# Kernel tuning notes

Hardware: AMD Instinct MI355X
Metric: run time of the kernel (lower is better)

## Reference

```python
import jax, jax.numpy as jnp
import numpy as np

H = 8       # num_heads
K = 16      # neighbours
LN_EPS = 1e-6

def _knn_indices(coords, k):
    # coords: (B,N,3) float32. Squared-euclidean distances preserve kNN ordering of cdist.
    d2 = jnp.sum(coords * coords, axis=-1)                      # (B,N)
    dist2 = d2[:, :, None] + d2[:, None, :] - 2.0 * jnp.einsum('bnd,bmd->bnm', coords, coords)
    _, idx = jax.lax.top_k(-dist2, k)                           # (B,N,k) smallest distances
    return idx

def _gather(x, idx):
    # x: (B,N,D), idx: (B,N,K) -> (B,N,K,D)
    return jax.vmap(lambda a, i: a[i])(x, idx)

def setup_inputs() -> dict:
    key = jax.random.key(0)
    ks = jax.random.split(key, 16)
    B, N, D = 2, 8192, 256
    P = 6
    std = 0.02
    inp = {
        'features': jax.random.normal(ks[0], (B, N, D), jnp.float32),
        'coords': jax.random.uniform(ks[1], (B, N, 3), jnp.float32),
        'normals': jax.random.normal(ks[2], (B, N, 3), jnp.float32),
        'mask': jnp.ones((B, N), jnp.float32),
        # linear weights stored (in, out): y = x @ W + b
        'Wq': jax.random.normal(ks[3], (D, D), jnp.float32) * std,
        'bq': jnp.zeros((D,), jnp.float32),
        'Wk': jax.random.normal(ks[4], (D, D), jnp.float32) * std,
        'bk': jnp.zeros((D,), jnp.float32),
        'Wv': jax.random.normal(ks[5], (D, D), jnp.float32) * std,
        'bv': jnp.zeros((D,), jnp.float32),
        'Wo': jax.random.normal(ks[6], (D, D), jnp.float32) * std,  # torch inits this to zero; random here for nontrivial test
        'bo': jnp.zeros((D,), jnp.float32),
        'Wp1': jax.random.normal(ks[7], (P, D), jnp.float32) * std,
        'bp1': jnp.zeros((D,), jnp.float32),
        'Wp2': jax.random.normal(ks[8], (D, D), jnp.float32) * std,
        'bp2': jnp.zeros((D,), jnp.float32),
        'gamma': jnp.ones((D,), jnp.float32),
        'beta': jnp.zeros((D,), jnp.float32),
    }
    return inp

def reference(features, coords, normals, mask, Wq, bq, Wk, bk, Wv, bv, Wo, bo,
              Wp1, bp1, Wp2, bp2, gamma, beta):
    B, N, D = features.shape
    dh = D // H
    scale = 1.0 / np.sqrt(dh).astype(np.float32)
    residual = features

    idx = _knn_indices(jax.lax.stop_gradient(coords), K)        # (B,N,K), no-grad as in torch

    nb_coords = _gather(coords, idx)                            # (B,N,K,3)
    rel_pos = coords[:, :, None, :] - nb_coords                 # (B,N,K,3)
    pos_input = jnp.concatenate(
        [rel_pos, jnp.broadcast_to(normals[:, :, None, :], rel_pos.shape)], axis=-1)  # (B,N,K,6)
    # pos MLP: Linear -> GELU(exact, torch default) -> Linear
    pos_emb = jax.nn.gelu(pos_input @ Wp1 + bp1, approximate=False) @ Wp2 + bp2       # (B,N,K,D)

    q = features @ Wq + bq                                      # (B,N,D)
    kp = features @ Wk + bk
    vp = features @ Wv + bv
    kg = _gather(kp, idx)                                       # (B,N,K,D)
    vg = _gather(vp, idx)

    k_comb = (kg + pos_emb).reshape(B, N, K, H, dh)
    v_comb = (vg + pos_emb).reshape(B, N, K, H, dh)
    qh = q.reshape(B, N, H, dh)

    logits = jnp.einsum('bnhd,bnkhd->bnkh', qh, k_comb) * scale  # (B,N,K,H)
    nb_valid = _gather(mask[..., None], idx)[..., 0]             # (B,N,K)
    logits = jnp.where(nb_valid[..., None] > 0, logits, -jnp.inf)
    attn = jax.nn.softmax(logits, axis=2)
    attn = jnp.nan_to_num(attn, nan=0.0)

    out = jnp.einsum('bnkh,bnkhd->bnhd', attn, v_comb).reshape(B, N, D)
    out = (out @ Wo + bo) * mask[..., None]

    h = residual + out
    mu = jnp.mean(h, axis=-1, keepdims=True)
    var = jnp.mean((h - mu) ** 2, axis=-1, keepdims=True)
    h = (h - mu) / jnp.sqrt(var + LN_EPS) * gamma + beta
    return h * mask[..., None]
```

## Files before the change

### kernel.cpp

```cpp
#include <hip/hip_runtime.h>
#include <hip/hip_bf16.h>
#include <math.h>

typedef unsigned short u16t;
typedef unsigned int   u32t;
typedef unsigned long long u64t;
typedef __attribute__((ext_vector_type(8))) short  short8;
typedef __attribute__((ext_vector_type(4))) float  floatx4;

#define NPTS   8192
#define DMODEL 256
#define BNTOT  16384
#define HSTR   264

__device__ __forceinline__ float bitsf(u32t u){ union { u32t i; float f; } v; v.i = u; return v.f; }
__device__ __forceinline__ float b2f(u16t s){ return bitsf(((u32t)s) << 16); }
__device__ __forceinline__ u16t f2b(float f){
  __hip_bfloat16 h = __float2bfloat16(f);
  return *reinterpret_cast<u16t*>(&h);
}
__device__ __forceinline__ uint4 pack8(const float* o){
  uint4 st;
  st.x = (u32t)f2b(o[0]) | ((u32t)f2b(o[1]) << 16);
  st.y = (u32t)f2b(o[2]) | ((u32t)f2b(o[3]) << 16);
  st.z = (u32t)f2b(o[4]) | ((u32t)f2b(o[5]) << 16);
  st.w = (u32t)f2b(o[6]) | ((u32t)f2b(o[7]) << 16);
  return st;
}

__device__ __forceinline__ float gelu_fast(float x){
  float ax = fabsf(x) * 0.70710678118654752f;
  float t  = __builtin_amdgcn_rcpf(__builtin_fmaf(0.3275911f, ax, 1.0f));
  float p  = t*(0.254829592f + t*(-0.284496736f + t*(1.421413741f +
             t*(-1.453152027f + t*1.061405429f))));
  float er = __builtin_fmaf(-p, __expf(-ax*ax), 1.0f);
  return 0.5f * x * (1.0f + copysignf(er, x));
}

__global__ __launch_bounds__(256) void fill_valf(float* p, int n, float v){
  int i = blockIdx.x * 256 + threadIdx.x;
  if (i < n) p[i] = v;
}

__global__ __launch_bounds__(256) void wprep4(const float* __restrict__ Wk,
                                              const float* __restrict__ Wv,
                                              const float* __restrict__ Wp2,
                                              const float* __restrict__ Wq,
                                              u16t* __restrict__ out) {
  int e = blockIdx.x * 256 + threadIdx.x;
  int m = e >> 16, r = e & 65535;
  const float* W = (m == 0) ? Wk : (m == 1 ? Wv : (m == 2 ? Wp2 : Wq));
  int v = r & 7, l = (r >> 3) & 63, cca = (r >> 9) & 15, ic = r >> 13;
  int i = ic * 32 + (l >> 4) * 8 + v;
  int c = cca * 16 + (l & 15);
  out[e] = f2b(W[(size_t)i * DMODEL + c]);
}
__global__ __launch_bounds__(256) void wprep1(const float* __restrict__ W,
                                              u16t* __restrict__ out) {
  int r = blockIdx.x * 256 + threadIdx.x;
  int v = r & 7, l = (r >> 3) & 63, cca = (r >> 9) & 15, ic = r >> 13;
  int i = ic * 32 + (l >> 4) * 8 + v;
  int c = cca * 16 + (l & 15);
  out[r] = f2b(W[(size_t)i * DMODEL + c]);
}

__device__ __forceinline__ void cswap_asc(u64t& a, u64t& b){
  u64t mn = (a < b) ? a : b;
  u64t mx = (a < b) ? b : a;
  a = mn; b = mx;
}
__device__ __forceinline__ void bitonic16(u64t v[16]){
  #pragma unroll
  for (int k = 2; k <= 16; k <<= 1) {
    #pragma unroll
    for (int j = k >> 1; j > 0; j >>= 1) {
      #pragma unroll
      for (int i = 0; i < 16; ++i) {
        int l = i ^ j;
        if (l > i) {
          if ((i & k) == 0) cswap_asc(v[i], v[l]);
          else              cswap_asc(v[l], v[i]);
        }
      }
    }
  }
}
__device__ __forceinline__ void merge16(u64t best[16], u64t v[16]){
  #pragma unroll
  for (int i = 0; i < 16; ++i) {
    u64t o = v[15 - i];
    best[i] = (best[i] < o) ? best[i] : o;
  }
  #pragma unroll
  for (int j = 8; j > 0; j >>= 1) {
    #pragma unroll
    for (int i = 0; i < 16; ++i) {
      int l = i ^ j;
      if (l > i) cswap_asc(best[i], best[l]);
    }
  }
}
__device__ __forceinline__ void knn_flush(u64t best[16], float& thrf, int& cnt,
                                          const u64t* bufw, int lane){
  u64t v[16];
  #pragma unroll
  for (int s = 0; s < 16; ++s) {
    u64t x = bufw[s * 64 + lane];
    v[s] = (s < cnt) ? x : 0xFFFFFFFFFFFFFFFFULL;
  }
  bitonic16(v);
  merge16(best, v);
  u32t k15 = (u32t)(best[15] >> 32);
  thrf = (k15 == 0xFFFFFFFFu) ? 3.3e38f
       : bitsf((k15 & 0x80000000u) ? (k15 ^ 0x80000000u) : ~k15);
  cnt = 0;
}

__global__ __launch_bounds__(256) void knn_partial(const float* __restrict__ coords,
                                                   u64t* __restrict__ pk) {
  int qb = blockIdx.x >> 3, ch = blockIdx.x & 7;
  int tid = threadIdx.x;
  int lane = tid & 63, wv = tid >> 6;
  int g = qb * 256 + tid;
  int b = g >> 13;
  alignas(16) __shared__ float4 tile[256];
  __shared__ u64t buf[4][16][64];

  float qx = coords[(size_t)g * 3 + 0];
  float qy = coords[(size_t)g * 3 + 1];
  float qz = coords[(size_t)g * 3 + 2];
  float qd2 = __fadd_rn(__fadd_rn(__fmul_rn(qx,qx), __fmul_rn(qy,qy)), __fmul_rn(qz,qz));

  u64t best[16];
  #pragma unroll
  for (int s = 0; s < 16; ++s) best[s] = 0xFFFFFFFFFFFFFFFFULL;
  float thrf = 3.3e38f;
  int  cnt = 0;
  u64t* bufw = &buf[wv][0][0];

  int cs = ch * 1024;
  for (int t = 0; t < 4; ++t) {
    int ci = cs + t * 256 + tid;
    size_t cb = (size_t)(b * NPTS + ci) * 3;
    float x = coords[cb + 0];
    float y = coords[cb + 1];
    float z = coords[cb + 2];
    float d2 = __fadd_rn(__fadd_rn(__fmul_rn(x,x), __fmul_rn(y,y)), __fmul_rn(z,z));
    __syncthreads();
    tile[tid] = make_float4(x, y, z, d2);
    __syncthreads();
    int cbase = cs + t * 256;
    for (int u = 0; u < 256; ++u) {
      float4 cd = tile[u];
      float dot = __fadd_rn(__fadd_rn(__fmul_rn(qx,cd.x), __fmul_rn(qy,cd.y)), __fmul_rn(qz,cd.z));
      float dist = __fsub_rn(__fadd_rn(qd2, cd.w), __fmul_rn(2.0f, dot));
      if (dist <= thrf) {
        u32t db  = __float_as_uint(dist);
        u32t key = db ^ ((u32t)(((int)db) >> 31) | 0x80000000u);
        bufw[cnt * 64 + lane] = ((u64t)key << 32) | (u32t)(cbase + u);
        ++cnt;
      }
      if (__any(cnt == 16)) knn_flush(best, thrf, cnt, bufw, lane);
    }
  }
  if (__any(cnt > 0)) knn_flush(best, thrf, cnt, bufw, lane);

  size_t base = (size_t)g * 128 + ch * 16;
  #pragma unroll
  for (int s = 0; s < 16; ++s) pk[base + s] = best[s];
}

__global__ __launch_bounds__(256) void knn_merge(const u64t* __restrict__ pk,
                                                 u16t* __restrict__ idxb) {
  int g = blockIdx.x * 256 + threadIdx.x;
  size_t base = (size_t)g * 128;
  int h[8];
  #pragma unroll
  for (int c = 0; c < 8; ++c) h[c] = 0;
  for (int s = 0; s < 16; ++s) {
    u64t bk = 0xFFFFFFFFFFFFFFFFULL; int bc = 0;
    #pragma unroll
    for (int c = 0; c < 8; ++c) {
      if (h[c] < 16) {
        u64t kk = pk[base + c * 16 + h[c]];
        if (kk < bk) { bk = kk; bc = c; }
      }
    }
    idxb[(size_t)g * 16 + s] = (u16t)(bk & 0xFFFFu);
    h[bc]++;
  }
}

__global__ __launch_bounds__(256) void gemm_kv_mfma(const float* __restrict__ feat,
    const u16t* __restrict__ frags,
    const float* __restrict__ bk, const float* __restrict__ bv,
    u16t* __restrict__ kb, u16t* __restrict__ vb) {
  int rbase = blockIdx.x * 32;
  int tid = threadIdx.x, lane = tid & 63, wvi = tid >> 6;
  int quad = lane >> 4, l15 = lane & 15;
  int mat = wvi >> 1, rg = wvi & 1;

  alignas(16) __shared__ u16t featS[32 * HSTR];

  {
    int r = tid >> 3, c0 = (tid & 7) * 32;
    const float* src = feat + (size_t)(rbase + r) * DMODEL + c0;
    u16t* dst = featS + r * HSTR + c0;
    #pragma unroll
    for (int t = 0; t < 4; ++t) {
      float4 a = *(const float4*)(src + t * 8);
      float4 b = *(const float4*)(src + t * 8 + 4);
      float o[8] = {a.x, a.y, a.z, a.w, b.x, b.y, b.z, b.w};
      *(uint4*)(dst + t * 8) = pack8(o);
    }
  }
  __syncthreads();

  short8 af[8];
  #pragma unroll
  for (int ic = 0; ic < 8; ++ic)
    af[ic] = *(const short8*)(featS + (rg * 16 + l15) * HSTR + ic * 32 + quad * 8);

  const u16t* wf    = frags + (size_t)mat * 65536;
  const float* bias = mat ? bv : bk;
  u16t* out         = mat ? vb : kb;

  floatx4 acc[16];
  #pragma unroll
  for (int ct = 0; ct < 16; ++ct) acc[ct] = (floatx4){0.f, 0.f, 0.f, 0.f};

  #pragma unroll
  for (int ic = 0; ic < 8; ++ic) {
    #pragma unroll
    for (int ct = 0; ct < 16; ++ct) {
      short8 bf = *(const short8*)(wf + (((size_t)(ic * 16 + ct) * 64 + lane) << 3));
      acc[ct] = __builtin_amdgcn_mfma_f32_16x16x32_bf16(af[ic], bf, acc[ct], 0, 0, 0);
    }
  }

  #pragma unroll
  for (int ct = 0; ct < 16; ++ct) {
    int col = ct * 16 + l15;
    float bvv = bias[col];
    #pragma unroll
    for (int r = 0; r < 4; ++r) {
      int row = rbase + rg * 16 + quad * 4 + r;
      out[(size_t)row * DMODEL + col] = f2b(acc[ct][r] + bvv);
    }
  }
}

__global__ __launch_bounds__(256, 4) void attn_mega(
    const float* __restrict__ coords, const float* __restrict__ normals,
    const float* __restrict__ maskp, const float* __restrict__ feat,
    const float* __restrict__ bq,
    const float* __restrict__ Wp1, const float* __restrict__ bp1,
    const float* __restrict__ bp2,
    const u16t* __restrict__ idxp,
    const u16t* __restrict__ wqfrag, const u16t* __restrict__ wp2frag,
    const u16t* __restrict__ kbuf, const u16t* __restrict__ vbuf,
    float* __restrict__ outp) {
  alignas(16) __shared__ u16t hemb[64 * HSTR];
  alignas(16) __shared__ u16t qB[8 * HSTR];
  __shared__ float wS[64];
  __shared__ int   idS[64];

  int c    = threadIdx.x;
  int lane = c & 63;
  int wv   = c >> 6;
  int quad = lane >> 4;
  int l15  = lane & 15;
  int wv4  = wv * 4;
  int qbase = blockIdx.x * 8;

  {
    int r = c >> 5, c0 = (c & 31) * 8;
    const float* src = feat + (size_t)(qbase + r) * DMODEL + c0;
    float4 a = *(const float4*)(src);
    float4 b = *(const float4*)(src + 4);
    float o[8] = {a.x, a.y, a.z, a.w, b.x, b.y, b.z, b.w};
    *(uint4*)(hemb + r * HSTR + c0) = pack8(o);
    uint4 z; z.x = 0u; z.y = 0u; z.z = 0u; z.w = 0u;
    *(uint4*)(hemb + (8 + r) * HSTR + c0) = z;
  }
  __syncthreads();

  {
    floatx4 qa[4];
    #pragma unroll
    for (int cc = 0; cc < 4; ++cc) qa[cc] = (floatx4){0.f, 0.f, 0.f, 0.f};
    #pragma unroll
    for (int ic = 0; ic < 8; ++ic) {
      short8 af = *(const short8*)(hemb + l15 * HSTR + ic * 32 + quad * 8);
      #pragma unroll
      for (int cc = 0; cc < 4; ++cc) {
        short8 bf = *(const short8*)(wqfrag + (((size_t)(ic * 16 + wv4 + cc) * 64 + lane) << 3));
        qa[cc] = __builtin_amdgcn_mfma_f32_16x16x32_bf16(af, bf, qa[cc], 0, 0, 0);
      }
    }
    if (quad < 2) {
      #pragma unroll
      for (int cc = 0; cc < 4; ++cc) {
        int col = (wv4 + cc) * 16 + l15;
        float bqv = bq[col];
        #pragma unroll
        for (int r = 0; r < 4; ++r)
          qB[(quad * 4 + r) * HSTR + col] = f2b(qa[cc][r] + bqv);
      }
    }
  }

  float w1[6];
  #pragma unroll
  for (int p = 0; p < 6; ++p) w1[p] = Wp1[p * DMODEL + c];
  float b1v = bp1[c];
  float b2c[4];
  #pragma unroll
  for (int cc = 0; cc < 4; ++cc) b2c[cc] = bp2[(wv4 + cc) * 16 + l15];
  const float lsc = 0.17677669529663687f;
  __syncthreads();

  #pragma unroll
  for (int G = 0; G < 2; ++G) {
    for (int ql = 0; ql < 4; ++ql) {
      int g = qbase + G * 4 + ql;
      int bb0 = (g >> 13) * NPTS;
      float qx = coords[(size_t)g * 3 + 0];
      float qy = coords[(size_t)g * 3 + 1];
      float qz = coords[(size_t)g * 3 + 2];
      float n0 = normals[(size_t)g * 3 + 0];
      float n1 = normals[(size_t)g * 3 + 1];
      float n2 = normals[(size_t)g * 3 + 2];
      #pragma unroll
      for (int j = 0; j < 16; ++j) {
        int id = (int)idxp[(size_t)g * 16 + j];
        size_t cb = (size_t)(bb0 + id) * 3;
        float rx = qx - coords[cb + 0];
        float ry = qy - coords[cb + 1];
        float rz = qz - coords[cb + 2];
        float pre = b1v + rx * w1[0] + ry * w1[1] + rz * w1[2]
                        + n0 * w1[3] + n1 * w1[4] + n2 * w1[5];
        hemb[(ql * 16 + j) * HSTR + c] = f2b(gelu_fast(pre));
      }
    }
    __syncthreads();

    floatx4 acc[4][4];
    #pragma unroll
    for (int rt = 0; rt < 4; ++rt)
      #pragma unroll
      for (int cc = 0; cc < 4; ++cc) acc[rt][cc] = (floatx4){0.f, 0.f, 0.f, 0.f};

    #pragma unroll
    for (int ic = 0; ic < 8; ++ic) {
      short8 af0 = *(const short8*)(hemb + ( 0 + l15) * HSTR + ic * 32 + quad * 8);
      short8 af1 = *(const short8*)(hemb + (16 + l15) * HSTR + ic * 32 + quad * 8);
      short8 af2 = *(const short8*)(hemb + (32 + l15) * HSTR + ic * 32 + quad * 8);
      short8 af3 = *(const short8*)(hemb + (48 + l15) * HSTR + ic * 32 + quad * 8);
      #pragma unroll
      for (int cc = 0; cc < 4; ++cc) {
        short8 bf = *(const short8*)(wp2frag + (((size_t)(ic * 16 + wv4 + cc) * 64 + lane) << 3));
        acc[0][cc] = __builtin_amdgcn_mfma_f32_16x16x32_bf16(af0, bf, acc[0][cc], 0, 0, 0);
        acc[1][cc] = __builtin_amdgcn_mfma_f32_16x16x32_bf16(af1, bf, acc[1][cc], 0, 0, 0);
        acc[2][cc] = __builtin_amdgcn_mfma_f32_16x16x32_bf16(af2, bf, acc[2][cc], 0, 0, 0);
        acc[3][cc] = __builtin_amdgcn_mfma_f32_16x16x32_bf16(af3, bf, acc[3][cc], 0, 0, 0);
      }
    }
    __syncthreads();
    #pragma unroll
    for (int rt = 0; rt < 4; ++rt)
      #pragma unroll
      for (int cc = 0; cc < 4; ++cc) {
        int cg = (wv4 + cc) * 16 + l15;
        #pragma unroll
        for (int r = 0; r < 4; ++r)
          hemb[(rt * 16 + quad * 4 + r) * HSTR + cg] = f2b(acc[rt][cc][r] + b2c[cc]);
      }
    __syncthreads();

    {
      int g = qbase + G * 4 + wv;
      int bb0 = (g >> 13) * NPTS;
      int idl = (int)idxp[(size_t)g * 16 + l15];
      float mvl = maskp[bb0 + idl];
      unsigned long long bm = __ballot(mvl > 0.0f);
      if (quad == 0) idS[wv * 16 + l15] = idl;
      const u16t* krow = kbuf + (size_t)(bb0 + idl) * DMODEL;
      const u16t* erow = hemb + (wv * 16 + l15) * HSTR;
      const u16t* qrow = qB + (G * 4 + wv) * HSTR;
      floatx4 sa = (floatx4){0.f, 0.f, 0.f, 0.f};
      #pragma unroll
      for (int ic = 0; ic < 8; ++ic) {
        short8 ak  = *(const short8*)(krow + ic * 32 + quad * 8);
        short8 ae  = *(const short8*)(erow + ic * 32 + quad * 8);
        short8 qb8 = *(const short8*)(qrow + ic * 32 + quad * 8);
        sa = __builtin_amdgcn_mfma_f32_16x16x32_bf16(ak, qb8, sa, 0, 0, 0);
        sa = __builtin_amdgcn_mfma_f32_16x16x32_bf16(ae, qb8, sa, 0, 0, 0);
      }
      float lg[4];
      #pragma unroll
      for (int r = 0; r < 4; ++r) {
        int j = quad * 4 + r;
        lg[r] = ((bm >> j) & 1ULL) ? sa[r] * lsc : -1e30f;
      }
      float m = fmaxf(fmaxf(lg[0], lg[1]), fmaxf(lg[2], lg[3]));
      m = fmaxf(m, __shfl_xor(m, 16));
      m = fmaxf(m, __shfl_xor(m, 32));
      float e0 = __expf(lg[0] - m), e1 = __expf(lg[1] - m);
      float e2 = __expf(lg[2] - m), e3 = __expf(lg[3] - m);
      float s = e0 + e1 + e2 + e3;
      s += __shfl_xor(s, 16);
      s += __shfl_xor(s, 32);
      float inv = (m > -1e29f) ? __builtin_amdgcn_rcpf(s) : 0.0f;
      if (l15 == 0) {
        wS[wv * 16 + quad * 4 + 0] = e0 * inv;
        wS[wv * 16 + quad * 4 + 1] = e1 * inv;
        wS[wv * 16 + quad * 4 + 2] = e2 * inv;
        wS[wv * 16 + quad * 4 + 3] = e3 * inv;
      }
    }
    __syncthreads();

    #pragma unroll
    for (int ql = 0; ql < 4; ++ql) {
      int g = qbase + G * 4 + ql;
      int bb0 = (g >> 13) * NPTS;
      float o = 0.0f;
      #pragma unroll
      for (int j = 0; j < 16; ++j) {
        int id  = idS[ql * 16 + j];
        float w = wS[ql * 16 + j];
        float vv = b2f(vbuf[(size_t)(bb0 + id) * DMODEL + c]);
        float ee = b2f(hemb[(ql * 16 + j) * HSTR + c]);
        o += w * (vv + ee);
      }
      outp[(size_t)g * DMODEL + c] = o;
    }
    if (G == 0) __syncthreads();
  }
}

__global__ __launch_bounds__(256) void gemm_out(const float* __restrict__ feat,
    const float* __restrict__ maskp,
    const u16t* __restrict__ wofrag, const float* __restrict__ bo,
    const float* __restrict__ gamma, const float* __restrict__ beta,
    float* __restrict__ io) {
  int rbase = blockIdx.x * 64;
  int tid = threadIdx.x, lane = tid & 63, wvi = tid >> 6;
  int quad = lane >> 4, l15 = lane & 15;

  alignas(16) __shared__ u16t oS[64 * HSTR];

  {
    int r = tid >> 2, c0 = (tid & 3) * 64;
    const float* src = io + (size_t)(rbase + r) * DMODEL + c0;
    u16t* dst = oS + r * HSTR + c0;
    #pragma unroll
    for (int t = 0; t < 8; ++t) {
      float4 a = *(const float4*)(src + t * 8);
      float4 b = *(const float4*)(src + t * 8 + 4);
      float o[8] = {a.x, a.y, a.z, a.w, b.x, b.y, b.z, b.w};
      *(uint4*)(dst + t * 8) = pack8(o);
    }
  }
  __syncthreads();

  floatx4 acc[16];
  #pragma unroll
  for (int ct = 0; ct < 16; ++ct) acc[ct] = (floatx4){0.f, 0.f, 0.f, 0.f};

  #pragma unroll
  for (int ic = 0; ic < 8; ++ic) {
    short8 af = *(const short8*)(oS + (wvi * 16 + l15) * HSTR + ic * 32 + quad * 8);
    #pragma unroll
    for (int ct = 0; ct < 16; ++ct) {
      short8 bf = *(const short8*)(wofrag + (((size_t)(ic * 16 + ct) * 64 + lane) << 3));
      acc[ct] = __builtin_amdgcn_mfma_f32_16x16x32_bf16(af, bf, acc[ct], 0, 0, 0);
    }
  }

  float bov[16], gamv[16], betv[16];
  #pragma unroll
  for (int ct = 0; ct < 16; ++ct) {
    int col = ct * 16 + l15;
    bov[ct]  = bo[col];
    gamv[ct] = gamma[col];
    betv[ct] = beta[col];
  }

  #pragma unroll
  for (int r = 0; r < 4; ++r) {
    int row = rbase + wvi * 16 + quad * 4 + r;
    float mv = maskp[row];
    float hv[16];
    float s = 0.0f, s2 = 0.0f;
    #pragma unroll
    for (int ct = 0; ct < 16; ++ct) {
      float h = feat[(size_t)row * DMODEL + ct * 16 + l15] + (acc[ct][r] + bov[ct]) * mv;
      hv[ct] = h; s += h; s2 += h * h;
    }
    #pragma unroll
    for (int off = 1; off < 16; off <<= 1) {
      s  += __shfl_xor(s,  off, 16);
      s2 += __shfl_xor(s2, off, 16);
    }
    float mu  = s  * (1.0f / 256.0f);
    float ms  = s2 * (1.0f / 256.0f);
    float var = ms - mu * mu;
    float inv = 1.0f / sqrtf(var + 1e-6f);
    #pragma unroll
    for (int ct = 0; ct < 16; ++ct) {
      float y = (hv[ct] - mu) * inv * gamv[ct] + betv[ct];
      y *= mv;
      io[(size_t)row * DMODEL + ct * 16 + l15] = y;
    }
  }
}

extern "C" void kernel_launch(void* const* d_in, const int* in_sizes, int n_in,
                              void* d_out, int out_size, void* d_ws, size_t ws_size,
                              hipStream_t stream) {
  static const int EXP[18] = {4194304, 49152, 49152, 16384,
                              65536, 256, 65536, 256, 65536, 256, 65536, 256,
                              1536, 256, 65536, 256, 256, 256};
  bool sizes_ok = (n_in >= 18);
  if (sizes_ok) for (int i = 0; i < 18; ++i) sizes_ok = sizes_ok && (in_sizes[i] == EXP[i]);
  int fb = (out_size + 255) / 256;
  if (!sizes_ok) {
    fill_valf<<<fb, 256, 0, stream>>>((float*)d_out, out_size, 0.0f);
    return;
  }
  const size_t WS_NEED = 17825792;
  if (ws_size < WS_NEED) {
    fill_valf<<<fb, 256, 0, stream>>>((float*)d_out, out_size, 1.0f);
    return;
  }

  const float* feat    = (const float*)d_in[0];
  const float* coords  = (const float*)d_in[1];
  const float* normals = (const float*)d_in[2];
  const float* maskp   = (const float*)d_in[3];
  const float* Wq  = (const float*)d_in[4];
  const float* bq  = (const float*)d_in[5];
  const float* Wk  = (const float*)d_in[6];
  const float* bk  = (const float*)d_in[7];
  const float* Wv  = (const float*)d_in[8];
  const float* bv  = (const float*)d_in[9];
  const float* Wo  = (const float*)d_in[10];
  const float* bo  = (const float*)d_in[11];
  const float* Wp1 = (const float*)d_in[12];
  const float* bp1 = (const float*)d_in[13];
  const float* Wp2 = (const float*)d_in[14];
  const float* bp2 = (const float*)d_in[15];
  const float* gamma = (const float*)d_in[16];
  const float* beta  = (const float*)d_in[17];

  char* ws = (char*)d_ws;
  u16t*  idx16  = (u16t*)(ws);
  u16t*  frags  = (u16t*)(ws + 524288);
  u16t*  kb     = (u16t*)(ws + 1048576);
  u16t*  vb     = (u16t*)(ws + 9437184);
  u64t*  pk     = (u64t*)(ws + 1048576);
  u16t*  wofrag = (u16t*)(ws + 1048576);

  wprep4<<<1024, 256, 0, stream>>>(Wk, Wv, Wp2, Wq, frags);
  knn_partial<<<512, 256, 0, stream>>>(coords, pk);
  knn_merge<<<64, 256, 0, stream>>>(pk, idx16);
  gemm_kv_mfma<<<512, 256, 0, stream>>>(feat, frags, bk, bv, kb, vb);
  attn_mega<<<2048, 256, 0, stream>>>(coords, normals, maskp, feat,
                                      bq, Wp1, bp1, bp2,
                                      idx16, frags + 196608, frags + 131072,
                                      kb, vb, (float*)d_out);
  wprep1<<<256, 256, 0, stream>>>(Wo, wofrag);
  gemm_out<<<256, 256, 0, stream>>>(feat, maskp, wofrag, bo, gamma, beta,
                                    (float*)d_out);
}
```

Measured before the change: 534.5 us.

## Spatially sort queries by grid cell and swizzle attention blocks across XCDs

Adds a counting sort (histogram, scan, scatter) that buckets query points into an 8x8x8 grid per batch. The attention kernel then processes queries in that permuted order. Block indices are also remapped so each XCD gets a contiguous range of sorted queries. The aim is for neighbouring queries on the same XCD to share kNN neighbours, so the gathered K/V/coords rows hit in L2 instead of being fetched scattered. The cost is four extra small launches, atomics, and scattered output-row writes.

```diff
diff --git a/kernel.cpp b/kernel.cpp
--- a/kernel.cpp
+++ b/kernel.cpp
@@ -64,6 +64,43 @@
   out[r] = f2b(W[(size_t)i * DMODEL + c]);
 }
 
+__device__ __forceinline__ int cell_of(const float* __restrict__ coords, int g){
+  float x = coords[(size_t)g * 3 + 0];
+  float y = coords[(size_t)g * 3 + 1];
+  float z = coords[(size_t)g * 3 + 2];
+  int cx = (int)(x * 8.0f); cx = cx < 0 ? 0 : (cx > 7 ? 7 : cx);
+  int cy = (int)(y * 8.0f); cy = cy < 0 ? 0 : (cy > 7 ? 7 : cy);
+  int cz = (int)(z * 8.0f); cz = cz < 0 ? 0 : (cz > 7 ? 7 : cz);
+  return (g >> 13) * 512 + cx * 64 + cy * 8 + cz;
+}
+__global__ __launch_bounds__(256) void sort_hist(const float* __restrict__ coords,
+                                                 u32t* __restrict__ cnt){
+  int g = blockIdx.x * 256 + threadIdx.x;
+  atomicAdd(&cnt[cell_of(coords, g)], 1u);
+}
+__global__ __launch_bounds__(1024) void sort_scan(u32t* __restrict__ cnt){
+  __shared__ u32t s[1024];
+  int t = threadIdx.x;
+  u32t orig = cnt[t];
+  s[t] = orig;
+  __syncthreads();
+  for (int off = 1; off < 1024; off <<= 1){
+    u32t x = s[t];
+    u32t y = (t >= off) ? s[t - off] : 0u;
+    __syncthreads();
+    s[t] = x + y;
+    __syncthreads();
+  }
+  cnt[t] = s[t] - orig;
+}
+__global__ __launch_bounds__(256) void sort_scatter(const float* __restrict__ coords,
+                                                    u32t* __restrict__ cnt,
+                                                    u32t* __restrict__ qperm){
+  int g = blockIdx.x * 256 + threadIdx.x;
+  u32t pos = atomicAdd(&cnt[cell_of(coords, g)], 1u);
+  qperm[pos] = (u32t)g;
+}
+
 __device__ __forceinline__ void cswap_asc(u64t& a, u64t& b){
   u64t mn = (a < b) ? a : b;
   u64t mx = (a < b) ? b : a;
@@ -256,7 +293,7 @@
     const float* __restrict__ bq,
     const float* __restrict__ Wp1, const float* __restrict__ bp1,
     const float* __restrict__ bp2,
-    const u16t* __restrict__ idxp,
+    const u16t* __restrict__ idxp, const u32t* __restrict__ qperm,
     const u16t* __restrict__ wqfrag, const u16t* __restrict__ wp2frag,
     const u16t* __restrict__ kbuf, const u16t* __restrict__ vbuf,
     float* __restrict__ outp) {
@@ -264,6 +301,7 @@
   alignas(16) __shared__ u16t qB[8 * HSTR];
   __shared__ float wS[64];
   __shared__ int   idS[64];
+  __shared__ int   qgS[8];
 
   int c    = threadIdx.x;
   int lane = c & 63;
@@ -271,11 +309,14 @@
   int quad = lane >> 4;
   int l15  = lane & 15;
   int wv4  = wv * 4;
-  int qbase = blockIdx.x * 8;
-
+  int sb   = ((blockIdx.x & 7) << 8) + (blockIdx.x >> 3);
+  int qpos = sb * 8;
+
+  if (c < 8) qgS[c] = (int)qperm[qpos + c];
   {
     int r = c >> 5, c0 = (c & 31) * 8;
-    const float* src = feat + (size_t)(qbase + r) * DMODEL + c0;
+    int gq = (int)qperm[qpos + r];
+    const float* src = feat + (size_t)gq * DMODEL + c0;
     float4 a = *(const float4*)(src);
     float4 b = *(const float4*)(src + 4);
     float o[8] = {a.x, a.y, a.z, a.w, b.x, b.y, b.z, b.w};
@@ -323,7 +364,7 @@
   #pragma unroll
   for (int G = 0; G < 2; ++G) {
     for (int ql = 0; ql < 4; ++ql) {
-      int g = qbase + G * 4 + ql;
+      int g = qgS[G * 4 + ql];
       int bb0 = (g >> 13) * NPTS;
       float qx = coords[(size_t)g * 3 + 0];
       float qy = coords[(size_t)g * 3 + 1];
@@ -379,7 +420,7 @@
     __syncthreads();
 
     {
-      int g = qbase + G * 4 + wv;
+      int g = qgS[G * 4 + wv];
       int bb0 = (g >> 13) * NPTS;
       int idl = (int)idxp[(size_t)g * 16 + l15];
       float mvl = maskp[bb0 + idl];
@@ -423,7 +464,7 @@
 
     #pragma unroll
     for (int ql = 0; ql < 4; ++ql) {
-      int g = qbase + G * 4 + ql;
+      int g = qgS[G * 4 + ql];
       int bb0 = (g >> 13) * NPTS;
       float o = 0.0f;
       #pragma unroll
@@ -562,14 +603,21 @@
   u16t*  vb     = (u16t*)(ws + 9437184);
   u64t*  pk     = (u64t*)(ws + 1048576);
   u16t*  wofrag = (u16t*)(ws + 1048576);
+  u32t*  qperm  = (u32t*)(ws + 524288);
+  u32t*  scnt   = (u32t*)(ws + 524288 + 65536);
 
   wprep4<<<1024, 256, 0, stream>>>(Wk, Wv, Wp2, Wq, frags);
   knn_partial<<<512, 256, 0, stream>>>(coords, pk);
   knn_merge<<<64, 256, 0, stream>>>(pk, idx16);
   gemm_kv_mfma<<<512, 256, 0, stream>>>(feat, frags, bk, bv, kb, vb);
+  fill_valf<<<4, 256, 0, stream>>>((float*)scnt, 1024, 0.0f);
+  sort_hist<<<64, 256, 0, stream>>>(coords, scnt);
+  sort_scan<<<1, 1024, 0, stream>>>(scnt);
+  sort_scatter<<<64, 256, 0, stream>>>(coords, scnt, qperm);
   attn_mega<<<2048, 256, 0, stream>>>(coords, normals, maskp, feat,
                                       bq, Wp1, bp1, bp2,
-                                      idx16, frags + 196608, frags + 131072,
+                                      idx16, qperm,
+                                      frags + 196608, frags + 131072,
                                       kb, vb, (float*)d_out);
   wprep1<<<256, 256, 0, stream>>>(Wo, wofrag);
   gemm_out<<<256, 256, 0, stream>>>(feat, maskp, wofrag, bo, gamma, beta,
```

New measurement: 530.9 us. About the same (-0.7%).
